# Performance work log

Measured on AMD Instinct MI355X. Metric: run time of the kernel, lower is better.

The kernel has to match this reference:

```python
import jax, jax.numpy as jnp
import numpy as np

D_MODEL, D_HIDDEN, N_EXPERTS = 1024, 4096, 8
CAP_FACTOR, LBL_COEF, ZLOSS_COEF = 1.25, 0.01, 0.0


def setup_inputs() -> dict:
    key = jax.random.key(0)
    ks = jax.random.split(key, 4)
    B, T = 4, 2048
    x = jax.random.normal(ks[0], (B, T, D_MODEL), dtype=jnp.float32)
    # router linear
    Wr = jax.random.normal(ks[1], (D_MODEL, N_EXPERTS), jnp.float32) / np.sqrt(D_MODEL).astype(np.float32)
    br = jnp.zeros((N_EXPERTS,), jnp.float32)
    # per-expert MLP: fc1 [D->H], gelu, fc2 [H->D]
    W1 = jax.random.normal(ks[2], (N_EXPERTS, D_MODEL, D_HIDDEN), jnp.float32) / np.sqrt(D_MODEL).astype(np.float32)
    b1 = jnp.zeros((N_EXPERTS, D_HIDDEN), jnp.float32)
    W2 = jax.random.normal(ks[3], (N_EXPERTS, D_HIDDEN, D_MODEL), jnp.float32) / np.sqrt(D_HIDDEN).astype(np.float32)
    b2 = jnp.zeros((N_EXPERTS, D_MODEL), jnp.float32)
    return {"x": x, "Wr": Wr, "br": br, "W1": W1, "b1": b1, "W2": W2, "b2": b2}


def reference(x, Wr, br, W1, b1, W2, b2):
    B, T, D = x.shape
    N = B * T
    E = Wr.shape[1]
    cap = int(CAP_FACTOR * (N / E) + 1)  # static Python int

    h = x.reshape(N, D)
    # --- Top1Router ---
    logits = h @ Wr + br                              # [N, E]
    probs = jax.nn.softmax(logits, axis=-1)
    top1 = jnp.argmax(probs, axis=-1)                 # [N]
    w = jnp.take_along_axis(probs, top1[:, None], axis=1)  # [N, 1]
    assign = jax.nn.one_hot(top1, E, dtype=jnp.float32)    # constant wrt grads
    importance = probs.mean(axis=0)
    load = jax.lax.stop_gradient(assign).mean(axis=0)
    lb_loss = E * jnp.sum(importance * load)
    z_loss = jnp.mean(jax.nn.logsumexp(logits, axis=-1) ** 2)

    # --- capacity-based dispatch (first `cap` tokens per expert, token order) ---
    pos = (jnp.cumsum(assign, axis=0) * assign).sum(axis=-1).astype(jnp.int32) - 1  # [N] slot within expert
    keep = pos < cap
    slot = jnp.where(keep, pos, cap)  # dropped tokens -> overflow slot `cap`
    xe = jnp.zeros((E, cap + 1, D), x.dtype).at[top1, slot].set(h)[:, :cap]  # [E, cap, D]

    # --- per-expert MLP as grouped GEMMs ---
    he = jax.nn.gelu(jnp.einsum('ecd,edh->ech', xe, W1) + b1[:, None, :])    # [E, cap, H]
    ye = jnp.einsum('ech,ehd->ecd', he, W2) + b2[:, None, :]                 # [E, cap, D]

    # --- combine (gather back, scale by router weight, zero dropped) ---
    out = ye[top1, jnp.minimum(pos, cap - 1)] * w   # [N, D]
    out = jnp.where(keep[:, None], out, jnp.zeros((), x.dtype))
    y = out.reshape(B, T, D)
    aux = LBL_COEF * lb_loss + ZLOSS_COEF * z_loss
    return (y, aux)
```

## Files before the change

### kernel.cpp

```cpp
#include <hip/hip_runtime.h>
#include <hip/hip_bf16.h>

#define N_TOK 8192
#define DM    1024
#define DH    4096
#define NE    8
#define CAP   1281
#define CAPR  1408
#define ISTR  1536

typedef unsigned short u16;
typedef __attribute__((ext_vector_type(8))) __bf16 bf16x8;
typedef __attribute__((ext_vector_type(8))) short short8;
typedef __attribute__((ext_vector_type(4))) short s16x4;
typedef __attribute__((ext_vector_type(4))) float f4;

__device__ __forceinline__ u16 f2bf(float f){
  union { float f; unsigned u; } v; v.f = f;
  unsigned r = v.u + 0x7fffu + ((v.u >> 16) & 1u);
  return (u16)(r >> 16);
}

__device__ __forceinline__ float gelu_fast(float v){
  float u = 0.7978845608028654f * (v + 0.044715f * v * v * v);
  return v * __builtin_amdgcn_rcpf(1.0f + __expf(-2.0f * u));
}

__device__ __forceinline__ void gl2lds16(const void* g, void* l){
  __builtin_amdgcn_global_load_lds((const __attribute__((address_space(1))) void*)g,
                                   (__attribute__((address_space(3))) void*)l, 16, 0, 0);
}

__global__ __launch_bounds__(256) void tcvt_k(const float* __restrict__ in, u16* __restrict__ out,
                                              int K, int Nn){
  __shared__ float tile[64][68];
  size_t mb = (size_t)blockIdx.z * (size_t)K * (size_t)Nn;
  const float* ip = in + mb;
  u16* op = out + mb;
  int n0 = blockIdx.x*64, k0 = blockIdx.y*64;
  int t = threadIdx.x;
  int kr = t>>4, nc = (t&15)*4;
  #pragma unroll
  for (int ii=0;ii<4;ii++){
    f4 v = *(const f4*)&ip[(size_t)(k0+kr+16*ii)*Nn + n0 + nc];
    tile[kr+16*ii][nc+0] = v[0]; tile[kr+16*ii][nc+1] = v[1];
    tile[kr+16*ii][nc+2] = v[2]; tile[kr+16*ii][nc+3] = v[3];
  }
  __syncthreads();
  int nr = t>>2, kc = (t&3)*16;
  short8 o0, o1;
  #pragma unroll
  for (int c=0;c<8;c++){
    o0[c] = (short)f2bf(tile[kc+c][nr]);
    o1[c] = (short)f2bf(tile[kc+8+c][nr]);
  }
  *(short8*)&op[(size_t)(n0+nr)*K + k0 + kc] = o0;
  *(short8*)&op[(size_t)(n0+nr)*K + k0 + kc + 8] = o1;
}

__global__ __launch_bounds__(256) void router_k(const float* __restrict__ x, const float* __restrict__ Wr,
    const float* __restrict__ br, u16* __restrict__ Xb, int* __restrict__ top1,
    float* __restrict__ wgt, float* __restrict__ impSum){
  __shared__ float pSh[4][8];
  int wid = threadIdx.x >> 6, lane = threadIdx.x & 63;
  int n = blockIdx.x * 4 + wid;
  const float* xr = x + (size_t)n * DM;
  u16* xbr = Xb + (size_t)n * DM;
  float acc[8];
  #pragma unroll
  for (int e=0;e<8;e++) acc[e]=0.f;
  #pragma unroll
  for (int c=0;c<4;c++){
    int d0 = c*256 + lane*4;
    f4 xv = *(const f4*)(xr + d0);
    s16x4 xb;
    #pragma unroll
    for (int j=0;j<4;j++) xb[j] = (short)f2bf(xv[j]);
    *(s16x4*)(xbr + d0) = xb;
    #pragma unroll
    for (int j=0;j<4;j++){
      const float* wrow = Wr + (size_t)(d0+j)*NE;
      float xs = xv[j];
      #pragma unroll
      for (int e=0;e<8;e++) acc[e] = fmaf(xs, wrow[e], acc[e]);
    }
  }
  #pragma unroll
  for (int off=32; off>0; off>>=1){
    #pragma unroll
    for (int e=0;e<8;e++) acc[e] += __shfl_down(acc[e], off, 64);
  }
  if (lane==0){
    float lg[8]; float mx = -1e30f;
    #pragma unroll
    for (int e=0;e<8;e++){ lg[e] = acc[e] + br[e]; mx = fmaxf(mx, lg[e]); }
    float p[8], s=0.f;
    #pragma unroll
    for (int e=0;e<8;e++){ p[e] = expf(lg[e]-mx); s += p[e]; }
    int bt=0; float bv=lg[0];
    #pragma unroll
    for (int e=1;e<8;e++){ if (lg[e]>bv){ bv=lg[e]; bt=e; } }
    float inv = 1.f/s;
    top1[n] = bt; wgt[n] = p[bt]*inv;
    #pragma unroll
    for (int e=0;e<8;e++) pSh[wid][e] = p[e]*inv;
  }
  __syncthreads();
  if (threadIdx.x < 8){
    int e = threadIdx.x;
    atomicAdd(&impSum[e], pSh[0][e]+pSh[1][e]+pSh[2][e]+pSh[3][e]);
  }
}

__global__ __launch_bounds__(1024) void scan_k(const int* __restrict__ top1, int* __restrict__ idx,
    int* __restrict__ cnt, int* __restrict__ dropList, int* __restrict__ nDrop,
    const float* __restrict__ impSum, float* __restrict__ auxOut){
  __shared__ int waveCnt[16][8];
  __shared__ int wavePre[16][8];
  __shared__ int chunkTot[8];
  __shared__ int base_s[8];
  int tid = threadIdx.x, wid = tid>>6, lane = tid&63;
  if (tid < 8) base_s[tid] = 0;
  __syncthreads();
  for (int c=0;c<8;c++){
    int t = c*1024 + tid;
    int e = top1[t];
    int myPre = 0;
    #pragma unroll
    for (int ex=0; ex<8; ex++){
      unsigned long long mk = __ballot(e == ex);
      if (lane == 0) waveCnt[wid][ex] = __popcll(mk);
      if (ex == e) myPre = __popcll(mk & ((1ull<<lane)-1ull));
    }
    __syncthreads();
    if (tid < 8){
      int run = 0;
      for (int wv=0; wv<16; wv++){ wavePre[wv][tid] = run; run += waveCnt[wv][tid]; }
      chunkTot[tid] = run;
    }
    __syncthreads();
    int pos = base_s[e] + wavePre[wid][e] + myPre;
    if (pos < CAP) idx[e*ISTR + pos] = t;
    else { int d = atomicAdd(nDrop, 1); dropList[d] = t; }
    __syncthreads();
    if (tid < 8) base_s[tid] += chunkTot[tid];
    __syncthreads();
  }
  if (tid < 8){
    cnt[tid] = base_s[tid] < CAP ? base_s[tid] : CAP;
  }
  if (tid == 0){
    float s = 0.f;
    for (int e=0;e<8;e++) s += (impSum[e]*(1.f/N_TOK)) * ((float)base_s[e]*(1.f/N_TOK));
    *auxOut = 0.01f * 8.f * s;
  }
}

__global__ __launch_bounds__(256) void zdrop_k(const int* __restrict__ dropList,
    const int* __restrict__ nDrop, float* __restrict__ y){
  int nd = *nDrop;
  for (int i = blockIdx.x; i < nd; i += gridDim.x){
    int t = dropList[i];
    f4* row = (f4*)(y + (size_t)t * DM);
    f4 z; z[0]=0.f; z[1]=0.f; z[2]=0.f; z[3]=0.f;
    row[threadIdx.x] = z;
  }
}

#define LDA(buf, m, kk) (*(const bf16x8*)&lds[(buf)*16384 + (aBase ^ ((kk)*32)) + (m)*1024])
#define LDB(buf, n, kk) (*(const bf16x8*)&lds[32768 + (buf)*16384 + (bBase ^ ((kk)*32)) + (n)*1024])

#define SA_J(buf, j, kc) gl2lds16(aS[j] + (size_t)(kc)*64, &lds[(buf)*16384 + ((j)*512 + t)*8])
#define SB_ALLM(buf, kc) do{ \
  gl2lds16(bS[0] + (size_t)(kc)*64, &lds[32768 + (buf)*16384 + (0*512 + t)*8]); \
  gl2lds16(bS[1] + (size_t)(kc)*64, &lds[32768 + (buf)*16384 + (1*512 + t)*8]); \
  gl2lds16(bS[2] + (size_t)(kc)*64, &lds[32768 + (buf)*16384 + (2*512 + t)*8]); \
  gl2lds16(bS[3] + (size_t)(kc)*64, &lds[32768 + (buf)*16384 + (3*512 + t)*8]); }while(0)

#define LGKM0 do{ asm volatile("s_waitcnt lgkmcnt(0)" ::: "memory"); \
                  __builtin_amdgcn_sched_barrier(0); }while(0)

#define MFMA_PAIR(q) \
  _Pragma("unroll") for (int j_=0;j_<2;j_++) \
    _Pragma("unroll") for (int n_=0;n_<4;n_++) \
      _Pragma("unroll") for (int kk_=0;kk_<2;kk_++) \
        acc[2*(q)+j_][n_] = __builtin_amdgcn_mfma_f32_16x16x32_bf16(a_[j_][kk_], Bf[n_][kk_], acc[2*(q)+j_][n_], 0,0,0);

#define KTILE(buf, ktv, NTv) do{ \
  int kc1 = (ktv)+1 < (NTv) ? (ktv)+1 : (NTv)-1; \
  int kc2 = (ktv)+2 < (NTv) ? (ktv)+2 : (NTv)-1; \
  bf16x8 a_[2][2]; \
  asm volatile("s_waitcnt vmcnt(6)" ::: "memory"); \
  __builtin_amdgcn_s_barrier(); \
  _Pragma("unroll") for (int n_=0;n_<4;n_++){ Bf[n_][0] = LDB(buf,n_,0); Bf[n_][1] = LDB(buf,n_,1); } \
  a_[0][0]=LDA(buf,0,0); a_[0][1]=LDA(buf,0,1); a_[1][0]=LDA(buf,1,0); a_[1][1]=LDA(buf,1,1); \
  SA_J((buf)^1, 1, kc1); SA_J((buf)^1, 3, kc1); \
  LGKM0; \
  __builtin_amdgcn_s_setprio(1); MFMA_PAIR(0); __builtin_amdgcn_s_setprio(0); \
  __builtin_amdgcn_s_barrier(); \
  a_[0][0]=LDA(buf,2,0); a_[0][1]=LDA(buf,2,1); a_[1][0]=LDA(buf,3,0); a_[1][1]=LDA(buf,3,1); \
  SB_ALLM(buf, kc2); \
  LGKM0; \
  __builtin_amdgcn_s_setprio(1); MFMA_PAIR(1); __builtin_amdgcn_s_setprio(0); \
  __builtin_amdgcn_s_barrier(); \
  a_[0][0]=LDA(buf,4,0); a_[0][1]=LDA(buf,4,1); a_[1][0]=LDA(buf,5,0); a_[1][1]=LDA(buf,5,1); \
  SA_J(buf, 0, kc2); SA_J(buf, 2, kc2); \
  LGKM0; \
  __builtin_amdgcn_s_setprio(1); MFMA_PAIR(2); __builtin_amdgcn_s_setprio(0); \
  __builtin_amdgcn_s_barrier(); \
  a_[0][0]=LDA(buf,6,0); a_[0][1]=LDA(buf,6,1); a_[1][0]=LDA(buf,7,0); a_[1][1]=LDA(buf,7,1); \
  LGKM0; \
  __builtin_amdgcn_s_setprio(1); MFMA_PAIR(3); __builtin_amdgcn_s_setprio(0); \
}while(0)

#define GEMM_PROLOGUE() do{ \
  SB_ALLM(0, 0); \
  SA_J(0,0,0); SA_J(0,2,0); \
  SA_J(0,1,0); SA_J(0,3,0); \
  SB_ALLM(1, 1); \
  SA_J(1,0,1); SA_J(1,2,1); }while(0)

__global__ __launch_bounds__(512, 2) void gemm1_k(
    const u16* __restrict__ Xb, const u16* __restrict__ W1T,
    const float* __restrict__ b1, const int* __restrict__ idx,
    const int* __restrict__ cnt, u16* __restrict__ He)
{
  int bid = blockIdx.x;
  int x = bid & 7, k = bid >> 3;
  int g = x*16 + k/6;
  int ntS = k - (k/6)*6;
  int e = g >> 4, mtH = g & 15;
  int cn = cnt[e];
  if (ntS*256 >= cn) return;
  __shared__ __align__(16) u16 lds[65536];
  int t = threadIdx.x, lane = t&63, wid = t>>6;
  int waveM = wid>>2, waveN = wid&3;
  int rA = lane&15, kb = lane>>4, s = rA&7;

  const u16* aS[4]; const u16* bS[4];
  #pragma unroll
  for (int j=0;j<4;j++){
    int pos = j*512 + t;
    int row = pos>>3, ch = pos&7;
    int gcb = ch ^ (row&7);
    aS[j] = W1T + ((size_t)e*DH + mtH*256 + row)*DM + gcb*8;
    int slotrow = ntS*256 + row;
    int token = (slotrow < cn) ? idx[e*ISTR + slotrow] : 0;
    bS[j] = Xb + (size_t)token*DM + gcb*8;
  }
  f4 acc[8][4];
  #pragma unroll
  for (int m=0;m<8;m++)
    #pragma unroll
    for (int n=0;n<4;n++)
      #pragma unroll
      for (int j=0;j<4;j++) acc[m][n][j]=0.f;

  int aBase = (waveM*128 + rA)*64 + (kb ^ s)*8;
  int bBase = (waveN*64  + rA)*64 + (kb ^ s)*8;
  bf16x8 Bf[4][2];

  GEMM_PROLOGUE();
  const int NT = DM/64;
  #pragma unroll 1
  for (int i=0;i<NT/2;i++){
    KTILE(0, 2*i,   NT);
    KTILE(1, 2*i+1, NT);
  }
  asm volatile("s_waitcnt vmcnt(0) lgkmcnt(0)" ::: "memory");

  int rG = lane>>4;
  #pragma unroll
  for (int m=0;m<8;m++){
    int h0 = mtH*256 + waveM*128 + m*16 + rG*4;
    f4 b4 = *(const f4*)&b1[e*DH + h0];
    #pragma unroll
    for (int n=0;n<4;n++){
      int slot = ntS*256 + waveN*64 + n*16 + rA;
      if (slot < cn){
        s16x4 v;
        #pragma unroll
        for (int j=0;j<4;j++) v[j] = (short)f2bf(gelu_fast(acc[m][n][j] + b4[j]));
        *(s16x4*)&He[((size_t)e*CAPR + slot)*DH + h0] = v;
      }
    }
  }
}

__global__ __launch_bounds__(512, 2) void gemm2_k(
    const u16* __restrict__ He, const u16* __restrict__ W2T,
    const float* __restrict__ b2, const int* __restrict__ idx,
    const int* __restrict__ cnt, const float* __restrict__ wgt,
    float* __restrict__ y)
{
  int bid = blockIdx.x;
  int x = bid & 7, k = bid >> 3;
  int g = x*4 + k/6;
  int mt = k - (k/6)*6;
  int e = g >> 2, nt = g & 3;
  int cn = cnt[e];
  if (mt*256 >= cn) return;
  __shared__ __align__(16) u16 lds[65536];
  int t = threadIdx.x, lane = t&63, wid = t>>6;
  int waveM = wid>>2, waveN = wid&3;
  int rA = lane&15, kb = lane>>4, s = rA&7;

  const u16* aS[4]; const u16* bS[4];
  #pragma unroll
  for (int j=0;j<4;j++){
    int pos = j*512 + t;
    int row = pos>>3, ch = pos&7;
    int gcb = ch ^ (row&7);
    int srow = mt*256 + row; if (srow >= cn) srow = cn-1;
    aS[j] = He  + ((size_t)e*CAPR + srow)*DH + gcb*8;
    bS[j] = W2T + ((size_t)e*DM + nt*256 + row)*DH + gcb*8;
  }
  f4 acc[8][4];
  #pragma unroll
  for (int m=0;m<8;m++)
    #pragma unroll
    for (int n=0;n<4;n++)
      #pragma unroll
      for (int j=0;j<4;j++) acc[m][n][j]=0.f;

  int aBase = (waveM*128 + rA)*64 + (kb ^ s)*8;
  int bBase = (waveN*64  + rA)*64 + (kb ^ s)*8;
  bf16x8 Bf[4][2];

  GEMM_PROLOGUE();
  const int NT = DH/64;
  #pragma unroll 1
  for (int i=0;i<NT/2;i++){
    KTILE(0, 2*i,   NT);
    KTILE(1, 2*i+1, NT);
  }
  asm volatile("s_waitcnt vmcnt(0) lgkmcnt(0)" ::: "memory");

  int rG = lane>>4;
  float bias_[4];
  #pragma unroll
  for (int n=0;n<4;n++) bias_[n] = b2[e*DM + nt*256 + waveN*64 + n*16 + rA];
  #pragma unroll
  for (int m=0;m<8;m++){
    int slot0 = mt*256 + waveM*128 + m*16 + rG*4;
    #pragma unroll
    for (int j=0;j<4;j++){
      int slot = slot0 + j;
      bool valid = slot < cn;
      int tk = valid ? idx[e*ISTR + slot] : 0;
      float wv = valid ? wgt[tk] : 0.f;
      float* yr = y + (size_t)tk*DM;
      #pragma unroll
      for (int n=0;n<4;n++){
        int col = nt*256 + waveN*64 + n*16 + rA;
        if (valid) yr[col] = (acc[m][n][j] + bias_[n]) * wv;
      }
    }
  }
}

extern "C" void kernel_launch(void* const* d_in, const int* in_sizes, int n_in,
                              void* d_out, int out_size, void* d_ws, size_t ws_size,
                              hipStream_t stream){
  const float* x  = (const float*)d_in[0];
  const float* Wr = (const float*)d_in[1];
  const float* br = (const float*)d_in[2];
  const float* W1 = (const float*)d_in[3];
  const float* b1 = (const float*)d_in[4];
  const float* W2 = (const float*)d_in[5];
  const float* b2 = (const float*)d_in[6];
  float* y = (float*)d_out;

  char* ws = (char*)d_ws;
  u16* Xb  = (u16*)(ws);
  u16* W1T = (u16*)(ws + 16777216ull);
  u16* W2T = (u16*)(ws + 16777216ull + 67108864ull);
  u16* He  = (u16*)(ws + 16777216ull + 2ull*67108864ull);
  char* tail = ws + 16777216ull + 2ull*67108864ull + (size_t)NE*CAPR*DH*2ull;
  int*   top1   = (int*)(tail);
  float* wgt    = (float*)(tail + 32768);
  int*   idx    = (int*)(tail + 65536);
  int*   drop   = (int*)(tail + 65536 + 49152);
  float* impSum = (float*)(tail + 65536 + 49152 + 32768);
  int*   nDrop  = (int*)((char*)impSum + 32);
  int*   cnt    = nDrop + 1;

  (void)hipMemsetAsync(impSum, 0, 64, stream);

  tcvt_k<<<dim3(64,16,8), 256, 0, stream>>>(W1, W1T, DM, DH);
  tcvt_k<<<dim3(16,64,8), 256, 0, stream>>>(W2, W2T, DH, DM);
  router_k<<<2048, 256, 0, stream>>>(x, Wr, br, Xb, top1, wgt, impSum);
  scan_k<<<1, 1024, 0, stream>>>(top1, idx, cnt, drop, nDrop, impSum,
                                 y + (size_t)N_TOK*DM);
  zdrop_k<<<64, 256, 0, stream>>>(drop, nDrop, y);
  gemm1_k<<<768, 512, 0, stream>>>(Xb, W1T, b1, idx, cnt, He);
  gemm2_k<<<192, 512, 0, stream>>>(He, W2T, b2, idx, cnt, wgt, y);

  (void)in_sizes; (void)n_in; (void)out_size; (void)ws_size;
}
```

Before: 348.4 us.

## Switch grouped GEMMs from 16x16x32 to 32x32x16 bf16 MFMA tiles

Both expert GEMM kernels now issue 32x32x16 MFMA instructions on 32-row fragments instead of 16x16x32 ones. The LDS read addressing, swizzle, fragment registers and epilogue index mapping are rewritten to match the 32x32 accumulator layout. Larger MFMA tiles cut the LDS fragment reads and instruction count per FLOP, raising arithmetic intensity per wave. The cost is a different register and LDS bank access pattern and a reworked epilogue, which adds risk of bank conflicts or register pressure.

```diff
diff --git a/kernel.cpp b/kernel.cpp
--- a/kernel.cpp
+++ b/kernel.cpp
@@ -14,6 +14,7 @@
 typedef __attribute__((ext_vector_type(8))) short short8;
 typedef __attribute__((ext_vector_type(4))) short s16x4;
 typedef __attribute__((ext_vector_type(4))) float f4;
+typedef __attribute__((ext_vector_type(16))) float f32x16;
 
 __device__ __forceinline__ u16 f2bf(float f){
   union { float f; unsigned u; } v; v.f = f;
@@ -167,8 +168,9 @@
   }
 }
 
-#define LDA(buf, m, kk) (*(const bf16x8*)&lds[(buf)*16384 + (aBase ^ ((kk)*32)) + (m)*1024])
-#define LDB(buf, n, kk) (*(const bf16x8*)&lds[32768 + (buf)*16384 + (bBase ^ ((kk)*32)) + (n)*1024])
+
+#define LDA32(buf, m, ks) (*(const bf16x8*)&lds[(buf)*16384 + aBase + (m)*2048 + ((((ks)*2+kb1))^s7)*8])
+#define LDB32(buf, n, ks) (*(const bf16x8*)&lds[32768 + (buf)*16384 + bBase + (n)*2048 + ((((ks)*2+kb1))^s7)*8])
 
 #define SA_J(buf, j, kc) gl2lds16(aS[j] + (size_t)(kc)*64, &lds[(buf)*16384 + ((j)*512 + t)*8])
 #define SB_ALLM(buf, kc) do{ \
@@ -177,40 +179,48 @@
   gl2lds16(bS[2] + (size_t)(kc)*64, &lds[32768 + (buf)*16384 + (2*512 + t)*8]); \
   gl2lds16(bS[3] + (size_t)(kc)*64, &lds[32768 + (buf)*16384 + (3*512 + t)*8]); }while(0)
 
-#define LGKM0 do{ asm volatile("s_waitcnt lgkmcnt(0)" ::: "memory"); \
-                  __builtin_amdgcn_sched_barrier(0); }while(0)
-
-#define MFMA_PAIR(q) \
-  _Pragma("unroll") for (int j_=0;j_<2;j_++) \
-    _Pragma("unroll") for (int n_=0;n_<4;n_++) \
-      _Pragma("unroll") for (int kk_=0;kk_<2;kk_++) \
-        acc[2*(q)+j_][n_] = __builtin_amdgcn_mfma_f32_16x16x32_bf16(a_[j_][kk_], Bf[n_][kk_], acc[2*(q)+j_][n_], 0,0,0);
+#define SB0 __builtin_amdgcn_sched_barrier(0)
+#define LGKM0 do{ asm volatile("s_waitcnt lgkmcnt(0)" ::: "memory"); SB0; }while(0)
+
+#define READ_A32(dst, mb, ksb, buf) do{ \
+  dst[0][0]=LDA32(buf,(mb),(ksb));   dst[0][1]=LDA32(buf,(mb),(ksb)+1); \
+  dst[1][0]=LDA32(buf,(mb)+1,(ksb)); dst[1][1]=LDA32(buf,(mb)+1,(ksb)+1); }while(0)
+
+#define MFMA8(ab, AF, kso) \
+  _Pragma("unroll") for (int ks_=0;ks_<2;ks_++) \
+    _Pragma("unroll") for (int mm_=0;mm_<2;mm_++) \
+      _Pragma("unroll") for (int n_=0;n_<2;n_++) \
+        acc[(ab)+mm_][n_] = __builtin_amdgcn_mfma_f32_32x32x16_bf16(AF[mm_][ks_], Bf[n_][(kso)+ks_], acc[(ab)+mm_][n_], 0,0,0);
 
 #define KTILE(buf, ktv, NTv) do{ \
   int kc1 = (ktv)+1 < (NTv) ? (ktv)+1 : (NTv)-1; \
   int kc2 = (ktv)+2 < (NTv) ? (ktv)+2 : (NTv)-1; \
-  bf16x8 a_[2][2]; \
+   \
   asm volatile("s_waitcnt vmcnt(6)" ::: "memory"); \
   __builtin_amdgcn_s_barrier(); \
-  _Pragma("unroll") for (int n_=0;n_<4;n_++){ Bf[n_][0] = LDB(buf,n_,0); Bf[n_][1] = LDB(buf,n_,1); } \
-  a_[0][0]=LDA(buf,0,0); a_[0][1]=LDA(buf,0,1); a_[1][0]=LDA(buf,1,0); a_[1][1]=LDA(buf,1,1); \
   SA_J((buf)^1, 1, kc1); SA_J((buf)^1, 3, kc1); \
+  _Pragma("unroll") for (int n_=0;n_<2;n_++) \
+    _Pragma("unroll") for (int k_=0;k_<4;k_++) Bf[n_][k_] = LDB32(buf,n_,k_); \
+  READ_A32(aA, 0, 0, buf); \
   LGKM0; \
-  __builtin_amdgcn_s_setprio(1); MFMA_PAIR(0); __builtin_amdgcn_s_setprio(0); \
+  __builtin_amdgcn_s_setprio(1); MFMA8(0, aA, 0); __builtin_amdgcn_s_setprio(0); \
+   \
   __builtin_amdgcn_s_barrier(); \
-  a_[0][0]=LDA(buf,2,0); a_[0][1]=LDA(buf,2,1); a_[1][0]=LDA(buf,3,0); a_[1][1]=LDA(buf,3,1); \
   SB_ALLM(buf, kc2); \
+  READ_A32(aB, 0, 2, buf); \
   LGKM0; \
-  __builtin_amdgcn_s_setprio(1); MFMA_PAIR(1); __builtin_amdgcn_s_setprio(0); \
+  __builtin_amdgcn_s_setprio(1); MFMA8(0, aB, 2); __builtin_amdgcn_s_setprio(0); \
+   \
   __builtin_amdgcn_s_barrier(); \
-  a_[0][0]=LDA(buf,4,0); a_[0][1]=LDA(buf,4,1); a_[1][0]=LDA(buf,5,0); a_[1][1]=LDA(buf,5,1); \
   SA_J(buf, 0, kc2); SA_J(buf, 2, kc2); \
+  READ_A32(aA, 2, 0, buf); \
   LGKM0; \
-  __builtin_amdgcn_s_setprio(1); MFMA_PAIR(2); __builtin_amdgcn_s_setprio(0); \
+  __builtin_amdgcn_s_setprio(1); MFMA8(2, aA, 0); __builtin_amdgcn_s_setprio(0); \
+   \
   __builtin_amdgcn_s_barrier(); \
-  a_[0][0]=LDA(buf,6,0); a_[0][1]=LDA(buf,6,1); a_[1][0]=LDA(buf,7,0); a_[1][1]=LDA(buf,7,1); \
+  READ_A32(aB, 2, 2, buf); \
   LGKM0; \
-  __builtin_amdgcn_s_setprio(1); MFMA_PAIR(3); __builtin_amdgcn_s_setprio(0); \
+  __builtin_amdgcn_s_setprio(1); MFMA8(2, aB, 2); __builtin_amdgcn_s_setprio(0); \
 }while(0)
 
 #define GEMM_PROLOGUE() do{ \
@@ -235,7 +245,7 @@
   __shared__ __align__(16) u16 lds[65536];
   int t = threadIdx.x, lane = t&63, wid = t>>6;
   int waveM = wid>>2, waveN = wid&3;
-  int rA = lane&15, kb = lane>>4, s = rA&7;
+  int rA5 = lane&31, kb1 = lane>>5, s7 = rA5&7;
 
   const u16* aS[4]; const u16* bS[4];
   #pragma unroll
@@ -248,17 +258,17 @@
     int token = (slotrow < cn) ? idx[e*ISTR + slotrow] : 0;
     bS[j] = Xb + (size_t)token*DM + gcb*8;
   }
-  f4 acc[8][4];
-  #pragma unroll
-  for (int m=0;m<8;m++)
-    #pragma unroll
-    for (int n=0;n<4;n++)
+  f32x16 acc[4][2];
+  #pragma unroll
+  for (int m=0;m<4;m++)
+    #pragma unroll
+    for (int n=0;n<2;n++)
       #pragma unroll
-      for (int j=0;j<4;j++) acc[m][n][j]=0.f;
-
-  int aBase = (waveM*128 + rA)*64 + (kb ^ s)*8;
-  int bBase = (waveN*64  + rA)*64 + (kb ^ s)*8;
-  bf16x8 Bf[4][2];
+      for (int j=0;j<16;j++) acc[m][n][j]=0.f;
+
+  int aBase = (waveM*128 + rA5)*64;
+  int bBase = (waveN*64  + rA5)*64;
+  bf16x8 Bf[2][4], aA[2][2], aB[2][2];
 
   GEMM_PROLOGUE();
   const int NT = DM/64;
@@ -269,19 +279,22 @@
   }
   asm volatile("s_waitcnt vmcnt(0) lgkmcnt(0)" ::: "memory");
 
-  int rG = lane>>4;
-  #pragma unroll
-  for (int m=0;m<8;m++){
-    int h0 = mtH*256 + waveM*128 + m*16 + rG*4;
-    f4 b4 = *(const f4*)&b1[e*DH + h0];
-    #pragma unroll
-    for (int n=0;n<4;n++){
-      int slot = ntS*256 + waveN*64 + n*16 + rA;
+  #pragma unroll
+  for (int m=0;m<4;m++){
+    #pragma unroll
+    for (int n=0;n<2;n++){
+      int slot = ntS*256 + waveN*64 + n*32 + rA5;
       if (slot < cn){
-        s16x4 v;
+        u16* dstrow = He + ((size_t)e*CAPR + slot)*DH;
         #pragma unroll
-        for (int j=0;j<4;j++) v[j] = (short)f2bf(gelu_fast(acc[m][n][j] + b4[j]));
-        *(s16x4*)&He[((size_t)e*CAPR + slot)*DH + h0] = v;
+        for (int q=0;q<4;q++){
+          int h0 = mtH*256 + waveM*128 + m*32 + q*8 + kb1*4;
+          f4 b4 = *(const f4*)&b1[e*DH + h0];
+          s16x4 v;
+          #pragma unroll
+          for (int j=0;j<4;j++) v[j] = (short)f2bf(gelu_fast(acc[m][n][q*4+j] + b4[j]));
+          *(s16x4*)&dstrow[h0] = v;
+        }
       }
     }
   }
@@ -303,7 +316,7 @@
   __shared__ __align__(16) u16 lds[65536];
   int t = threadIdx.x, lane = t&63, wid = t>>6;
   int waveM = wid>>2, waveN = wid&3;
-  int rA = lane&15, kb = lane>>4, s = rA&7;
+  int rA5 = lane&31, kb1 = lane>>5, s7 = rA5&7;
 
   const u16* aS[4]; const u16* bS[4];
   #pragma unroll
@@ -315,17 +328,17 @@
     aS[j] = He  + ((size_t)e*CAPR + srow)*DH + gcb*8;
     bS[j] = W2T + ((size_t)e*DM + nt*256 + row)*DH + gcb*8;
   }
-  f4 acc[8][4];
-  #pragma unroll
-  for (int m=0;m<8;m++)
-    #pragma unroll
-    for (int n=0;n<4;n++)
+  f32x16 acc[4][2];
+  #pragma unroll
+  for (int m=0;m<4;m++)
+    #pragma unroll
+    for (int n=0;n<2;n++)
       #pragma unroll
-      for (int j=0;j<4;j++) acc[m][n][j]=0.f;
-
-  int aBase = (waveM*128 + rA)*64 + (kb ^ s)*8;
-  int bBase = (waveN*64  + rA)*64 + (kb ^ s)*8;
-  bf16x8 Bf[4][2];
+      for (int j=0;j<16;j++) acc[m][n][j]=0.f;
+
+  int aBase = (waveM*128 + rA5)*64;
+  int bBase = (waveN*64  + rA5)*64;
+  bf16x8 Bf[2][4], aA[2][2], aB[2][2];
 
   GEMM_PROLOGUE();
   const int NT = DH/64;
@@ -336,24 +349,25 @@
   }
   asm volatile("s_waitcnt vmcnt(0) lgkmcnt(0)" ::: "memory");
 
-  int rG = lane>>4;
-  float bias_[4];
-  #pragma unroll
-  for (int n=0;n<4;n++) bias_[n] = b2[e*DM + nt*256 + waveN*64 + n*16 + rA];
-  #pragma unroll
-  for (int m=0;m<8;m++){
-    int slot0 = mt*256 + waveM*128 + m*16 + rG*4;
-    #pragma unroll
-    for (int j=0;j<4;j++){
-      int slot = slot0 + j;
-      bool valid = slot < cn;
-      int tk = valid ? idx[e*ISTR + slot] : 0;
-      float wv = valid ? wgt[tk] : 0.f;
-      float* yr = y + (size_t)tk*DM;
+  float bias_[2];
+  #pragma unroll
+  for (int n=0;n<2;n++) bias_[n] = b2[e*DM + nt*256 + waveN*64 + n*32 + rA5];
+  #pragma unroll
+  for (int m=0;m<4;m++){
+    #pragma unroll
+    for (int q=0;q<4;q++){
       #pragma unroll
-      for (int n=0;n<4;n++){
-        int col = nt*256 + waveN*64 + n*16 + rA;
-        if (valid) yr[col] = (acc[m][n][j] + bias_[n]) * wv;
+      for (int j=0;j<4;j++){
+        int slot = mt*256 + waveM*128 + m*32 + q*8 + kb1*4 + j;
+        bool valid = slot < cn;
+        int tk = valid ? idx[e*ISTR + slot] : 0;
+        float wv = valid ? wgt[tk] : 0.f;
+        float* yr = y + (size_t)tk*DM;
+        #pragma unroll
+        for (int n=0;n<2;n++){
+          int col = nt*256 + waveN*64 + n*32 + rA5;
+          if (valid) yr[col] = (acc[m][n][q*4+j] + bias_[n]) * wv;
+        }
       }
     }
   }
```

New measurement: 385.1 us. 10.5% more time.
